# Kernel optimization log

Measured on AMD Instinct MI355X. Metric: run time of the kernel, lower is better.

The kernel has to match this reference:

```python
import jax, jax.numpy as jnp
import numpy as np

N = 50000       # nodes
E = 800000      # edges
D_IN = 128
D_OUT = 128
K = 3           # num_stacks
T = 2           # num_layers


def setup_inputs() -> dict:
    key = jax.random.key(0)
    ks = jax.random.split(key, 10)
    feats = jax.random.normal(ks[0], (N, D_IN), dtype=jnp.float32)
    src = jax.random.randint(ks[1], (E,), 0, N, dtype=jnp.int32)
    dst = jax.random.randint(ks[2], (E,), 0, N, dtype=jnp.int32)
    s = 0.05
    w0 = jax.random.normal(ks[3], (K, D_IN, D_OUT), dtype=jnp.float32) * s
    b0 = jax.random.normal(ks[4], (K, D_OUT), dtype=jnp.float32) * s
    w = jax.random.normal(ks[5], (K, D_OUT, D_OUT), dtype=jnp.float32) * s
    bw = jax.random.normal(ks[6], (K, D_OUT), dtype=jnp.float32) * s
    v = jax.random.normal(ks[7], (K, D_IN, D_OUT), dtype=jnp.float32) * s
    bv = jax.random.normal(ks[8], (K, D_OUT), dtype=jnp.float32) * s
    return {"feats": feats, "src": src, "dst": dst,
            "w0": w0, "b0": b0, "w": w, "bw": bw, "v": v, "bv": bv}


def _propagate(h, src, dst, norm):
    # symmetric degree-normalized SpMM: D^{-1/2} A D^{-1/2} h
    h = h * norm                                   # [N, d]
    agg = jax.ops.segment_sum(h[src], dst, num_segments=N)  # gather + scatter-add
    return agg * norm


def reference(feats, src, dst, w0, b0, w, bw, v, bv):
    ones = jnp.ones((E,), dtype=feats.dtype)
    deg = jnp.clip(jax.ops.segment_sum(ones, dst, num_segments=N), 1.0)
    norm = (deg ** -0.5)[:, None]                  # [N, 1]

    out = jnp.zeros((N, D_OUT), dtype=feats.dtype)
    for k in range(K):
        h = feats
        for t in range(T):
            h = _propagate(h, src, dst, norm)
            if t == 0:
                h = h @ w0[k] + b0[k]
            else:
                h = h @ w[k] + bw[k]
            h = h + (feats @ v[k] + bv[k])         # dropout is identity (p=0, eval)
            h = jax.nn.relu(h)
        out = out + h
    return out / K
```

## Files before the change

kernel.cpp:

```cpp
#include <hip/hip_runtime.h>

#define N_NODES 50000
#define N_EDGES 800000
#define D 128
#define PLANE ((size_t)N_NODES * D)
#define NCHUNK ((N_NODES + 255) / 256)

typedef float f32x4 __attribute__((ext_vector_type(4)));
typedef float f32x2 __attribute__((ext_vector_type(2)));
typedef short bf16x8 __attribute__((ext_vector_type(8)));

__device__ __forceinline__ unsigned short f2bf(float x) {
  unsigned int u = __float_as_uint(x);
  u += 0x7FFFu + ((u >> 16) & 1u);
  return (unsigned short)(u >> 16);
}
__device__ __forceinline__ float bf2f(unsigned short h) {
  return __uint_as_float((unsigned int)h << 16);
}
__device__ __forceinline__ unsigned char f32_to_fp8(float x) {
  int p = __builtin_amdgcn_cvt_pk_fp8_f32(x, x, 0, false);
  return (unsigned char)(p & 0xFF);
}
__device__ __forceinline__ void fp8x4_to_f32(int pk, float* f) {
  f32x2 lo = __builtin_amdgcn_cvt_pk_f32_fp8(pk, false);
  f32x2 hi = __builtin_amdgcn_cvt_pk_f32_fp8(pk, true);
  f[0] = lo.x; f[1] = lo.y; f[2] = hi.x; f[3] = hi.y;
}


__global__ __launch_bounds__(256) void scan_local(const int* __restrict__ cnt,
                                                  int* __restrict__ local,
                                                  int* __restrict__ partial) {
  __shared__ int s[256];
  int t = threadIdx.x;
  int i = blockIdx.x * 256 + t;
  int v = (i < N_NODES) ? cnt[i] : 0;
  s[t] = v;
  __syncthreads();
  for (int off = 1; off < 256; off <<= 1) {
    int tmp = (t >= off) ? s[t - off] : 0;
    __syncthreads();
    s[t] += tmp;
    __syncthreads();
  }
  if (i < N_NODES) local[i] = s[t] - v;
  if (t == 255) partial[blockIdx.x] = s[255];
}

__global__ __launch_bounds__(256) void scan_chunks(const int* __restrict__ partial,
                                                   int* __restrict__ chunk_off,
                                                   int* __restrict__ rowptr) {
  __shared__ int s[256];
  int t = threadIdx.x;
  int v = (t < NCHUNK) ? partial[t] : 0;
  s[t] = v;
  __syncthreads();
  for (int off = 1; off < 256; off <<= 1) {
    int tmp = (t >= off) ? s[t - off] : 0;
    __syncthreads();
    s[t] += tmp;
    __syncthreads();
  }
  if (t < NCHUNK) chunk_off[t] = s[t] - v;
  if (t == 255) rowptr[N_NODES] = s[255];
}

__global__ __launch_bounds__(256) void finalize_rows(const int* __restrict__ cnt,
                                                     const int* __restrict__ local,
                                                     const int* __restrict__ chunk_off,
                                                     int* __restrict__ rowptr,
                                                     int* __restrict__ cursor,
                                                     float* __restrict__ norm) {
  int i = blockIdx.x * 256 + threadIdx.x;
  if (i < N_NODES) {
    int r = local[i] + chunk_off[blockIdx.x];
    rowptr[i] = r;
    cursor[i] = r;
    int d = cnt[i];
    if (d < 1) d = 1;
    norm[i] = rsqrtf((float)d);
  }
}

__global__ __launch_bounds__(256) void fill_csr(const int* __restrict__ src,
                                                const int* __restrict__ dst,
                                                int* __restrict__ cursor,
                                                int* __restrict__ col) {
  int e = blockIdx.x * blockDim.x + threadIdx.x;
  if (e < N_EDGES) {
    int pos = atomicAdd(&cursor[dst[e]], 1);
    col[pos] = src[e];
  }
}


#define CONV_THREADS ((int)(PLANE / 4))
#define WT_THREADS (2 * 3 * 128 * 256)
#define PREP_TOTAL (CONV_THREADS + WT_THREADS + N_EDGES)

__global__ __launch_bounds__(256) void prep_all(const float* __restrict__ feats,
                                                const float* __restrict__ w0,
                                                const float* __restrict__ w,
                                                const float* __restrict__ v,
                                                const int* __restrict__ dst,
                                                unsigned short* __restrict__ feats_bf,
                                                unsigned char* __restrict__ feats_fp8,
                                                unsigned short* __restrict__ bt_h1,
                                                unsigned short* __restrict__ bt_out,
                                                int* __restrict__ cnt) {
  int idx = blockIdx.x * 256 + threadIdx.x;
  if (idx < CONV_THREADS) {
    float4 x = ((const float4*)feats)[idx];
    ushort4 o;
    o.x = f2bf(x.x);
    o.y = f2bf(x.y);
    o.z = f2bf(x.z);
    o.w = f2bf(x.w);
    ((ushort4*)feats_bf)[idx] = o;
    int p = __builtin_amdgcn_cvt_pk_fp8_f32(x.x, x.y, 0, false);
    p = __builtin_amdgcn_cvt_pk_fp8_f32(x.z, x.w, p, true);
    ((int*)feats_fp8)[idx] = p;
    return;
  }
  idx -= CONV_THREADS;
  if (idx < WT_THREADS) {
    int buf = idx / 98304;
    int rem = idx - buf * 98304;
    int stack = rem / 32768;
    int rem2 = rem & 32767;
    int n = rem2 >> 8;
    int k = rem2 & 255;
    const float* srcm;
    int kk;
    if (k < 128) {
      srcm = (buf == 0) ? w0 : w;
      kk = k;
    } else {
      srcm = v;
      kk = k - 128;
    }
    float val = srcm[(size_t)stack * 16384 + (size_t)kk * 128 + n];
    unsigned short* dstb = (buf == 0) ? bt_h1 : bt_out;
    dstb[(size_t)stack * 32768 + (size_t)n * 256 + k] = f2bf(val);
    return;
  }
  idx -= WT_THREADS;
  if (idx < N_EDGES) atomicAdd(&cnt[dst[idx]], 1);
}


template <int NK>
__global__ __launch_bounds__(256) void spmm_fp8(const unsigned char* __restrict__ h,
                                                const float* __restrict__ norm,
                                                const int* __restrict__ rowptr,
                                                const int* __restrict__ col,
                                                unsigned short* __restrict__ out) {
  int row = blockIdx.x * 4 + (threadIdx.x >> 6);
  if (row >= N_NODES) return;
  int lane = threadIdx.x & 63;
  int sub = lane >> 3;
  int c8 = lane & 7;
  int beg = rowptr[row], end = rowptr[row + 1];

  float acc[NK][16];
#pragma unroll
  for (int m = 0; m < NK; ++m)
#pragma unroll
    for (int j = 0; j < 16; ++j) acc[m][j] = 0.f;

#pragma unroll 2
  for (int e = beg; e < end; e += 8) {
    int eidx = e + sub;
    bool valid = eidx < end;
    int s = valid ? col[eidx] : 0;
    float wgt = valid ? norm[s] : 0.f;
    const unsigned char* hp = h + (size_t)s * D + c8 * 16;
#pragma unroll
    for (int m = 0; m < NK; ++m) {
      int4 pkt = *(const int4*)(hp + m * PLANE);
      float f[16];
      fp8x4_to_f32(pkt.x, f + 0);
      fp8x4_to_f32(pkt.y, f + 4);
      fp8x4_to_f32(pkt.z, f + 8);
      fp8x4_to_f32(pkt.w, f + 12);
#pragma unroll
      for (int j = 0; j < 16; ++j) acc[m][j] = fmaf(wgt, f[j], acc[m][j]);
    }
  }

#pragma unroll
  for (int m = 0; m < NK; ++m)
#pragma unroll
    for (int j = 0; j < 16; ++j) {
      float vv = acc[m][j];
      vv += __shfl_xor(vv, 8);
      vv += __shfl_xor(vv, 16);
      vv += __shfl_xor(vv, 32);
      acc[m][j] = vv;
    }

  if (sub == 0) {
    float nd = norm[row];
#pragma unroll
    for (int m = 0; m < NK; ++m) {
      bf16x8 o0, o1;
#pragma unroll
      for (int j = 0; j < 8; ++j) {
        o0[j] = (short)f2bf(acc[m][j] * nd);
        o1[j] = (short)f2bf(acc[m][j + 8] * nd);
      }
      unsigned short* op = out + m * PLANE + (size_t)row * D + c8 * 16;
      *(bf16x8*)op = o0;
      *(bf16x8*)(op + 8) = o1;
    }
  }
}


__device__ __forceinline__ void stage_B64(unsigned short (*Bs)[256],
                                          const unsigned short* __restrict__ Btg,
                                          int nh, int tid) {
#pragma unroll
  for (int i = 0; i < 8; ++i) {
    int t = tid + i * 256;
    int n = t >> 5;
    int kc = t & 31;
    int kcs = kc ^ (n & 31);
    *(bf16x8*)&Bs[n][kcs * 8] = *(const bf16x8*)(Btg + (size_t)(nh + n) * 256 + kc * 8);
  }
}

__device__ __forceinline__ bf16x8 read_B64(const unsigned short (*Bs)[256], int n,
                                           int chunk) {
  return *(const bf16x8*)&Bs[n][(chunk ^ (n & 31)) * 8];
}

__global__ __launch_bounds__(256) void gemm_h1_fused(
    const unsigned short* __restrict__ P,
    const unsigned short* __restrict__ feats_bf,
    const unsigned short* __restrict__ Bt,
    const float* __restrict__ b0, const float* __restrict__ bv,
    unsigned char* __restrict__ h1_fp8) {
  __shared__ unsigned short Bs[64][256];
  int nh = blockIdx.y * 64;

  int tid = threadIdx.x;
  int lane = tid & 63;
  int wv = tid >> 6;
  int ln15 = lane & 15;
  int g = lane >> 4;

  int m0 = blockIdx.x * 128 + wv * 32;
  int r0 = m0 + ln15;
  int r1 = m0 + 16 + ln15;
  if (r0 >= N_NODES) r0 = N_NODES - 1;
  if (r1 >= N_NODES) r1 = N_NODES - 1;

  bf16x8 a0[8], a1[8];
#pragma unroll
  for (int s = 0; s < 4; ++s) {
    a0[s] = *(const bf16x8*)(P + (size_t)r0 * 128 + g * 8 + s * 32);
    a1[s] = *(const bf16x8*)(P + (size_t)r1 * 128 + g * 8 + s * 32);
    a0[s + 4] = *(const bf16x8*)(feats_bf + (size_t)r0 * 128 + g * 8 + s * 32);
    a1[s + 4] = *(const bf16x8*)(feats_bf + (size_t)r1 * 128 + g * 8 + s * 32);
  }

  for (int stk = 0; stk < 3; ++stk) {
    if (stk) __syncthreads();
    stage_B64(Bs, Bt + (size_t)stk * 32768, nh, tid);
    __syncthreads();

    f32x4 acc0[4], acc1[4];
#pragma unroll
    for (int nt = 0; nt < 4; ++nt) { acc0[nt] = (f32x4)(0.f); acc1[nt] = (f32x4)(0.f); }

#pragma unroll
    for (int s = 0; s < 8; ++s) {
#pragma unroll
      for (int nt = 0; nt < 4; ++nt) {
        bf16x8 bfr = read_B64(Bs, nt * 16 + ln15, s * 4 + g);
        acc0[nt] = __builtin_amdgcn_mfma_f32_16x16x32_bf16(a0[s], bfr, acc0[nt], 0, 0, 0);
        acc1[nt] = __builtin_amdgcn_mfma_f32_16x16x32_bf16(a1[s], bfr, acc1[nt], 0, 0, 0);
      }
    }

    unsigned char* outp = h1_fp8 + (size_t)stk * PLANE;
#pragma unroll
    for (int nt = 0; nt < 4; ++nt) {
      int colj = nh + nt * 16 + ln15;
      float bsum = b0[stk * 128 + colj] + bv[stk * 128 + colj];
#pragma unroll
      for (int r = 0; r < 4; ++r) {
        int mA = m0 + g * 4 + r;
        int mB = m0 + 16 + g * 4 + r;
        if (mA < N_NODES) {
          float x = acc0[nt][r] + bsum;
          outp[(size_t)mA * 128 + colj] = f32_to_fp8(x > 0.f ? x : 0.f);
        }
        if (mB < N_NODES) {
          float x = acc1[nt][r] + bsum;
          outp[(size_t)mB * 128 + colj] = f32_to_fp8(x > 0.f ? x : 0.f);
        }
      }
    }
  }
}

__global__ __launch_bounds__(256) void gemm_out_fused(
    const unsigned short* __restrict__ agg,
    const unsigned short* __restrict__ feats_bf,
    const unsigned short* __restrict__ Bt,
    const float* __restrict__ bwp, const float* __restrict__ bvp,
    float* __restrict__ outp) {
  __shared__ unsigned short Bs[64][256];
  int nh = blockIdx.y * 64;

  int tid = threadIdx.x;
  int lane = tid & 63;
  int wv = tid >> 6;
  int ln15 = lane & 15;
  int g = lane >> 4;

  int m0 = blockIdx.x * 128 + wv * 32;
  int r0 = m0 + ln15;
  int r1 = m0 + 16 + ln15;
  if (r0 >= N_NODES) r0 = N_NODES - 1;
  if (r1 >= N_NODES) r1 = N_NODES - 1;

  bf16x8 f0[4], f1[4];
#pragma unroll
  for (int s = 0; s < 4; ++s) {
    f0[s] = *(const bf16x8*)(feats_bf + (size_t)r0 * 128 + g * 8 + s * 32);
    f1[s] = *(const bf16x8*)(feats_bf + (size_t)r1 * 128 + g * 8 + s * 32);
  }

  f32x4 sum0[4], sum1[4];
#pragma unroll
  for (int nt = 0; nt < 4; ++nt) { sum0[nt] = (f32x4)(0.f); sum1[nt] = (f32x4)(0.f); }

  for (int stk = 0; stk < 3; ++stk) {
    if (stk) __syncthreads();
    stage_B64(Bs, Bt + (size_t)stk * 32768, nh, tid);
    __syncthreads();

    const unsigned short* A1 = agg + (size_t)stk * PLANE;
    bf16x8 g0[4], g1[4];
#pragma unroll
    for (int s = 0; s < 4; ++s) {
      g0[s] = *(const bf16x8*)(A1 + (size_t)r0 * 128 + g * 8 + s * 32);
      g1[s] = *(const bf16x8*)(A1 + (size_t)r1 * 128 + g * 8 + s * 32);
    }

    f32x4 acc0[4], acc1[4];
#pragma unroll
    for (int nt = 0; nt < 4; ++nt) { acc0[nt] = (f32x4)(0.f); acc1[nt] = (f32x4)(0.f); }

#pragma unroll
    for (int s = 0; s < 8; ++s) {
      bf16x8 af0 = (s < 4) ? g0[s & 3] : f0[s & 3];
      bf16x8 af1 = (s < 4) ? g1[s & 3] : f1[s & 3];
#pragma unroll
      for (int nt = 0; nt < 4; ++nt) {
        bf16x8 bfr = read_B64(Bs, nt * 16 + ln15, s * 4 + g);
        acc0[nt] = __builtin_amdgcn_mfma_f32_16x16x32_bf16(af0, bfr, acc0[nt], 0, 0, 0);
        acc1[nt] = __builtin_amdgcn_mfma_f32_16x16x32_bf16(af1, bfr, acc1[nt], 0, 0, 0);
      }
    }

#pragma unroll
    for (int nt = 0; nt < 4; ++nt) {
      int colj = nh + nt * 16 + ln15;
      float bsum = bwp[stk * 128 + colj] + bvp[stk * 128 + colj];
#pragma unroll
      for (int r = 0; r < 4; ++r) {
        float x0 = acc0[nt][r] + bsum;
        float x1 = acc1[nt][r] + bsum;
        sum0[nt][r] += (x0 > 0.f ? x0 : 0.f);
        sum1[nt][r] += (x1 > 0.f ? x1 : 0.f);
      }
    }
  }

  const float sc = 1.0f / 3.0f;
#pragma unroll
  for (int nt = 0; nt < 4; ++nt) {
    int colj = nh + nt * 16 + ln15;
#pragma unroll
    for (int r = 0; r < 4; ++r) {
      int mA = m0 + g * 4 + r;
      int mB = m0 + 16 + g * 4 + r;
      if (mA < N_NODES) outp[(size_t)mA * 128 + colj] = sum0[nt][r] * sc;
      if (mB < N_NODES) outp[(size_t)mB * 128 + colj] = sum1[nt][r] * sc;
    }
  }
}


extern "C" void kernel_launch(void* const* d_in, const int* in_sizes, int n_in,
                              void* d_out, int out_size, void* d_ws, size_t ws_size,
                              hipStream_t stream) {
  const float* feats = (const float*)d_in[0];
  const int* src = (const int*)d_in[1];
  const int* dst = (const int*)d_in[2];
  const float* w0 = (const float*)d_in[3];
  const float* b0 = (const float*)d_in[4];
  const float* w = (const float*)d_in[5];
  const float* bw = (const float*)d_in[6];
  const float* v = (const float*)d_in[7];
  const float* bv = (const float*)d_in[8];
  float* out = (float*)d_out;

  char* ws = (char*)d_ws;
  size_t off = 0;
  auto alloc = [&](size_t bytes) {
    void* p = ws + off;
    off += (bytes + 255) & ~(size_t)255;
    return p;
  };
  int* cnt = (int*)alloc(N_NODES * 4);
  int* local = (int*)alloc(N_NODES * 4);
  int* partial = (int*)alloc(NCHUNK * 4);
  int* chunk_off = (int*)alloc(NCHUNK * 4);
  float* norm = (float*)alloc(N_NODES * 4);
  int* rowptr = (int*)alloc((N_NODES + 1) * 4);
  int* cursor = (int*)alloc(N_NODES * 4);
  int* col = (int*)alloc(N_EDGES * 4);
  unsigned short* bt_h1 = (unsigned short*)alloc(3 * 32768 * 2);
  unsigned short* bt_out = (unsigned short*)alloc(3 * 32768 * 2);

  size_t pb = PLANE * 2;
  unsigned short* feats_bf = (unsigned short*)alloc(pb);
  unsigned char* feats_fp8 = (unsigned char*)alloc(PLANE);
  unsigned short* P_bf = (unsigned short*)alloc(pb);
  unsigned char* h1_fp8 = (unsigned char*)alloc(3 * PLANE);
  unsigned short* agg_bf = (unsigned short*)alloc(3 * pb);

  hipMemsetAsync(cnt, 0, N_NODES * 4, stream);

  dim3 blk(256);
  prep_all<<<(PREP_TOTAL + 255) / 256, blk, 0, stream>>>(feats, w0, w, v, dst, feats_bf,
                                                         feats_fp8, bt_h1, bt_out, cnt);
  scan_local<<<NCHUNK, blk, 0, stream>>>(cnt, local, partial);
  scan_chunks<<<1, blk, 0, stream>>>(partial, chunk_off, rowptr);
  finalize_rows<<<NCHUNK, blk, 0, stream>>>(cnt, local, chunk_off, rowptr, cursor, norm);
  fill_csr<<<(N_EDGES + 255) / 256, blk, 0, stream>>>(src, dst, cursor, col);

  int sblocks = (N_NODES + 3) / 4;
  int mblocks = (N_NODES + 127) / 128;
  dim3 ggrid(mblocks, 2);

  spmm_fp8<1><<<sblocks, blk, 0, stream>>>(feats_fp8, norm, rowptr, col, P_bf);
  gemm_h1_fused<<<ggrid, blk, 0, stream>>>(P_bf, feats_bf, bt_h1, b0, bv, h1_fp8);
  spmm_fp8<3><<<sblocks, blk, 0, stream>>>(h1_fp8, norm, rowptr, col, agg_bf);
  gemm_out_fused<<<ggrid, blk, 0, stream>>>(agg_bf, feats_bf, bt_out, bw, bv, out);
}
```

Before: 353.7 us.

## Prescale sources by norm, interleave stack planes per node, persistent SpMM waves

The source-side degree normalization now happens when the fp8 inputs are produced: in prep_all for the features and in the h1 GEMM epilogue. This removes the per-edge norm[s] gather from the SpMM inner loop. The h1 buffer is laid out node-major with all three stacks contiguous per node, so one gathered row covers 384 bytes instead of three separate planes. The SpMM becomes a grid-stride loop over a fixed 2048 blocks, and degree counting moves into its own kernel so the norm is ready before prep. This adds one kernel launch and quantizes the values after the norm scaling rather than before.

```diff
diff --git a/kernel.cpp b/kernel.cpp
--- a/kernel.cpp
+++ b/kernel.cpp
@@ -28,6 +28,12 @@
   f[0] = lo.x; f[1] = lo.y; f[2] = hi.x; f[3] = hi.y;
 }
 
+
+__global__ __launch_bounds__(256) void count_deg(const int* __restrict__ dst,
+                                                 int* __restrict__ cnt) {
+  int e = blockIdx.x * blockDim.x + threadIdx.x;
+  if (e < N_EDGES) atomicAdd(&cnt[dst[e]], 1);
+}
 
 __global__ __launch_bounds__(256) void scan_local(const int* __restrict__ cnt,
                                                   int* __restrict__ local,
@@ -97,18 +103,17 @@
 
 #define CONV_THREADS ((int)(PLANE / 4))
 #define WT_THREADS (2 * 3 * 128 * 256)
-#define PREP_TOTAL (CONV_THREADS + WT_THREADS + N_EDGES)
+#define PREP_TOTAL (CONV_THREADS + WT_THREADS)
 
 __global__ __launch_bounds__(256) void prep_all(const float* __restrict__ feats,
                                                 const float* __restrict__ w0,
                                                 const float* __restrict__ w,
                                                 const float* __restrict__ v,
-                                                const int* __restrict__ dst,
+                                                const float* __restrict__ norm,
                                                 unsigned short* __restrict__ feats_bf,
                                                 unsigned char* __restrict__ feats_fp8,
                                                 unsigned short* __restrict__ bt_h1,
-                                                unsigned short* __restrict__ bt_out,
-                                                int* __restrict__ cnt) {
+                                                unsigned short* __restrict__ bt_out) {
   int idx = blockIdx.x * 256 + threadIdx.x;
   if (idx < CONV_THREADS) {
     float4 x = ((const float4*)feats)[idx];
@@ -118,35 +123,32 @@
     o.z = f2bf(x.z);
     o.w = f2bf(x.w);
     ((ushort4*)feats_bf)[idx] = o;
-    int p = __builtin_amdgcn_cvt_pk_fp8_f32(x.x, x.y, 0, false);
-    p = __builtin_amdgcn_cvt_pk_fp8_f32(x.z, x.w, p, true);
+    float nd = norm[idx >> 5];
+    int p = __builtin_amdgcn_cvt_pk_fp8_f32(x.x * nd, x.y * nd, 0, false);
+    p = __builtin_amdgcn_cvt_pk_fp8_f32(x.z * nd, x.w * nd, p, true);
     ((int*)feats_fp8)[idx] = p;
     return;
   }
   idx -= CONV_THREADS;
-  if (idx < WT_THREADS) {
-    int buf = idx / 98304;
-    int rem = idx - buf * 98304;
-    int stack = rem / 32768;
-    int rem2 = rem & 32767;
-    int n = rem2 >> 8;
-    int k = rem2 & 255;
-    const float* srcm;
-    int kk;
-    if (k < 128) {
-      srcm = (buf == 0) ? w0 : w;
-      kk = k;
-    } else {
-      srcm = v;
-      kk = k - 128;
-    }
-    float val = srcm[(size_t)stack * 16384 + (size_t)kk * 128 + n];
-    unsigned short* dstb = (buf == 0) ? bt_h1 : bt_out;
-    dstb[(size_t)stack * 32768 + (size_t)n * 256 + k] = f2bf(val);
-    return;
-  }
-  idx -= WT_THREADS;
-  if (idx < N_EDGES) atomicAdd(&cnt[dst[idx]], 1);
+  if (idx >= WT_THREADS) return;
+  int buf = idx / 98304;
+  int rem = idx - buf * 98304;
+  int stack = rem / 32768;
+  int rem2 = rem & 32767;
+  int n = rem2 >> 8;
+  int k = rem2 & 255;
+  const float* srcm;
+  int kk;
+  if (k < 128) {
+    srcm = (buf == 0) ? w0 : w;
+    kk = k;
+  } else {
+    srcm = v;
+    kk = k - 128;
+  }
+  float val = srcm[(size_t)stack * 16384 + (size_t)kk * 128 + n];
+  unsigned short* dstb = (buf == 0) ? bt_h1 : bt_out;
+  dstb[(size_t)stack * 32768 + (size_t)n * 256 + k] = f2bf(val);
 }
 
 
@@ -156,63 +158,66 @@
                                                 const int* __restrict__ rowptr,
                                                 const int* __restrict__ col,
                                                 unsigned short* __restrict__ out) {
-  int row = blockIdx.x * 4 + (threadIdx.x >> 6);
-  if (row >= N_NODES) return;
+  int wave = blockIdx.x * 4 + (threadIdx.x >> 6);
+  int nwaves = gridDim.x * 4;
   int lane = threadIdx.x & 63;
   int sub = lane >> 3;
   int c8 = lane & 7;
-  int beg = rowptr[row], end = rowptr[row + 1];
-
-  float acc[NK][16];
-#pragma unroll
-  for (int m = 0; m < NK; ++m)
-#pragma unroll
-    for (int j = 0; j < 16; ++j) acc[m][j] = 0.f;
+
+  for (int row = wave; row < N_NODES; row += nwaves) {
+    int beg = rowptr[row], end = rowptr[row + 1];
+
+    float acc[NK][16];
+#pragma unroll
+    for (int m = 0; m < NK; ++m)
+#pragma unroll
+      for (int j = 0; j < 16; ++j) acc[m][j] = 0.f;
 
 #pragma unroll 2
-  for (int e = beg; e < end; e += 8) {
-    int eidx = e + sub;
-    bool valid = eidx < end;
-    int s = valid ? col[eidx] : 0;
-    float wgt = valid ? norm[s] : 0.f;
-    const unsigned char* hp = h + (size_t)s * D + c8 * 16;
-#pragma unroll
-    for (int m = 0; m < NK; ++m) {
-      int4 pkt = *(const int4*)(hp + m * PLANE);
-      float f[16];
-      fp8x4_to_f32(pkt.x, f + 0);
-      fp8x4_to_f32(pkt.y, f + 4);
-      fp8x4_to_f32(pkt.z, f + 8);
-      fp8x4_to_f32(pkt.w, f + 12);
-#pragma unroll
-      for (int j = 0; j < 16; ++j) acc[m][j] = fmaf(wgt, f[j], acc[m][j]);
-    }
-  }
-
-#pragma unroll
-  for (int m = 0; m < NK; ++m)
-#pragma unroll
-    for (int j = 0; j < 16; ++j) {
-      float vv = acc[m][j];
-      vv += __shfl_xor(vv, 8);
-      vv += __shfl_xor(vv, 16);
-      vv += __shfl_xor(vv, 32);
-      acc[m][j] = vv;
-    }
-
-  if (sub == 0) {
-    float nd = norm[row];
-#pragma unroll
-    for (int m = 0; m < NK; ++m) {
-      bf16x8 o0, o1;
-#pragma unroll
-      for (int j = 0; j < 8; ++j) {
-        o0[j] = (short)f2bf(acc[m][j] * nd);
-        o1[j] = (short)f2bf(acc[m][j + 8] * nd);
-      }
-      unsigned short* op = out + m * PLANE + (size_t)row * D + c8 * 16;
-      *(bf16x8*)op = o0;
-      *(bf16x8*)(op + 8) = o1;
+    for (int e = beg; e < end; e += 8) {
+      int eidx = e + sub;
+      bool valid = eidx < end;
+      int s = valid ? col[eidx] : 0;
+      float msk = valid ? 1.f : 0.f;
+      const unsigned char* hp = h + (size_t)s * (NK * 128) + c8 * 16;
+#pragma unroll
+      for (int m = 0; m < NK; ++m) {
+        int4 pkt = *(const int4*)(hp + m * 128);
+        float f[16];
+        fp8x4_to_f32(pkt.x, f + 0);
+        fp8x4_to_f32(pkt.y, f + 4);
+        fp8x4_to_f32(pkt.z, f + 8);
+        fp8x4_to_f32(pkt.w, f + 12);
+#pragma unroll
+        for (int j = 0; j < 16; ++j) acc[m][j] = fmaf(msk, f[j], acc[m][j]);
+      }
+    }
+
+#pragma unroll
+    for (int m = 0; m < NK; ++m)
+#pragma unroll
+      for (int j = 0; j < 16; ++j) {
+        float vv = acc[m][j];
+        vv += __shfl_xor(vv, 8);
+        vv += __shfl_xor(vv, 16);
+        vv += __shfl_xor(vv, 32);
+        acc[m][j] = vv;
+      }
+
+    if (sub == 0) {
+      float nd = norm[row];
+#pragma unroll
+      for (int m = 0; m < NK; ++m) {
+        bf16x8 o0, o1;
+#pragma unroll
+        for (int j = 0; j < 8; ++j) {
+          o0[j] = (short)f2bf(acc[m][j] * nd);
+          o1[j] = (short)f2bf(acc[m][j + 8] * nd);
+        }
+        unsigned short* op = out + m * PLANE + (size_t)row * D + c8 * 16;
+        *(bf16x8*)op = o0;
+        *(bf16x8*)(op + 8) = o1;
+      }
     }
   }
 }
@@ -241,6 +246,7 @@
     const unsigned short* __restrict__ feats_bf,
     const unsigned short* __restrict__ Bt,
     const float* __restrict__ b0, const float* __restrict__ bv,
+    const float* __restrict__ norm,
     unsigned char* __restrict__ h1_fp8) {
   __shared__ unsigned short Bs[64][256];
   int nh = blockIdx.y * 64;
@@ -285,7 +291,6 @@
       }
     }
 
-    unsigned char* outp = h1_fp8 + (size_t)stk * PLANE;
 #pragma unroll
     for (int nt = 0; nt < 4; ++nt) {
       int colj = nh + nt * 16 + ln15;
@@ -296,11 +301,13 @@
         int mB = m0 + 16 + g * 4 + r;
         if (mA < N_NODES) {
           float x = acc0[nt][r] + bsum;
-          outp[(size_t)mA * 128 + colj] = f32_to_fp8(x > 0.f ? x : 0.f);
+          x = (x > 0.f ? x : 0.f) * norm[mA];
+          h1_fp8[((size_t)mA * 3 + stk) * 128 + colj] = f32_to_fp8(x);
         }
         if (mB < N_NODES) {
           float x = acc1[nt][r] + bsum;
-          outp[(size_t)mB * 128 + colj] = f32_to_fp8(x > 0.f ? x : 0.f);
+          x = (x > 0.f ? x : 0.f) * norm[mB];
+          h1_fp8[((size_t)mB * 3 + stk) * 128 + colj] = f32_to_fp8(x);
         }
       }
     }
@@ -439,19 +446,20 @@
   hipMemsetAsync(cnt, 0, N_NODES * 4, stream);
 
   dim3 blk(256);
-  prep_all<<<(PREP_TOTAL + 255) / 256, blk, 0, stream>>>(feats, w0, w, v, dst, feats_bf,
-                                                         feats_fp8, bt_h1, bt_out, cnt);
+  count_deg<<<(N_EDGES + 255) / 256, blk, 0, stream>>>(dst, cnt);
   scan_local<<<NCHUNK, blk, 0, stream>>>(cnt, local, partial);
   scan_chunks<<<1, blk, 0, stream>>>(partial, chunk_off, rowptr);
   finalize_rows<<<NCHUNK, blk, 0, stream>>>(cnt, local, chunk_off, rowptr, cursor, norm);
   fill_csr<<<(N_EDGES + 255) / 256, blk, 0, stream>>>(src, dst, cursor, col);
-
-  int sblocks = (N_NODES + 3) / 4;
+  prep_all<<<(PREP_TOTAL + 255) / 256, blk, 0, stream>>>(feats, w0, w, v, norm, feats_bf,
+                                                         feats_fp8, bt_h1, bt_out);
+
+  int sblocks = 2048;
   int mblocks = (N_NODES + 127) / 128;
   dim3 ggrid(mblocks, 2);
 
   spmm_fp8<1><<<sblocks, blk, 0, stream>>>(feats_fp8, norm, rowptr, col, P_bf);
-  gemm_h1_fused<<<ggrid, blk, 0, stream>>>(P_bf, feats_bf, bt_h1, b0, bv, h1_fp8);
+  gemm_h1_fused<<<ggrid, blk, 0, stream>>>(P_bf, feats_bf, bt_h1, b0, bv, norm, h1_fp8);
   spmm_fp8<3><<<sblocks, blk, 0, stream>>>(h1_fp8, norm, rowptr, col, agg_bf);
   gemm_out_fused<<<ggrid, blk, 0, stream>>>(agg_bf, feats_bf, bt_out, bw, bv, out);
 }
```

New measurement: 380.3 us. +7.5%, slower.
